# Kernel optimization log

Hardware: AMD Instinct MI355X
Metric: run time of the kernel (lower is better)

The kernel has to match this reference:

```python
import jax, jax.numpy as jnp
import numpy as np

B = 32        # number of groups (batch.unique())
L = 512       # max_len (equal-size groups in this setup)
E = 512       # embed_dim
H = 8         # num_heads
N = B * L


def setup_inputs() -> dict:
    key = jax.random.key(0)
    k1, k2, k3 = jax.random.split(key, 3)
    embeddings = jax.random.normal(k1, (N, E), dtype=jnp.float32)
    # sorted group ids; equal group sizes keep max_len static for jit
    batch = jnp.repeat(jnp.arange(B, dtype=jnp.int32), L)
    in_proj_w = jax.random.normal(k2, (3 * E, E), dtype=jnp.float32) * (1.0 / np.sqrt(E))
    in_proj_b = jnp.zeros((3 * E,), dtype=jnp.float32)
    out_proj_w = jax.random.normal(k3, (E, E), dtype=jnp.float32) * (1.0 / np.sqrt(E))
    out_proj_b = jnp.zeros((E,), dtype=jnp.float32)
    return {"embeddings": embeddings, "batch": batch,
            "in_proj_w": in_proj_w, "in_proj_b": in_proj_b,
            "out_proj_w": out_proj_w, "out_proj_b": out_proj_b}


def reference(embeddings, batch, in_proj_w, in_proj_b, out_proj_w, out_proj_b):
    Dh = E // H
    ones = jnp.ones_like(batch, dtype=jnp.int32)
    counts = jax.ops.segment_sum(ones, batch, num_segments=B)          # [B]
    starts = jnp.cumsum(counts) - counts                               # exclusive cumsum
    pos = jnp.arange(N, dtype=jnp.int32) - starts[batch]               # position within group
    # pad ragged -> [B, L, E] (zeros for padding, as in torch code)
    padded = jnp.zeros((B, L, E), dtype=embeddings.dtype).at[batch, pos].set(embeddings)
    # FAITHFUL float attn_mask: +1.0 added to scores outside the valid block
    valid = (jnp.arange(L)[None, :] < counts[:, None]).astype(embeddings.dtype)  # [B, L]
    add_mask = 1.0 - valid[:, :, None] * valid[:, None, :]             # [B, Lq, Lk]

    qkv = padded @ in_proj_w.T + in_proj_b                             # [B, L, 3E]
    q, k, v = jnp.split(qkv, 3, axis=-1)
    q = q.reshape(B, L, H, Dh)
    k = k.reshape(B, L, H, Dh)
    v = v.reshape(B, L, H, Dh)
    scale = 1.0 / np.sqrt(Dh)
    scores = jnp.einsum('bqhd,bkhd->bhqk', q, k) * scale + add_mask[:, None, :, :]
    attn = jax.nn.softmax(scores, axis=-1)
    ctx = jnp.einsum('bhqk,bkhd->bqhd', attn, v).reshape(B, L, E)
    attn_out = ctx @ out_proj_w.T + out_proj_b                         # [B, L, E]
    # max_pool1d over sequence (includes padded query rows, as original)
    return jnp.max(attn_out, axis=1)                                   # [B, E]
```

## Files before the change

kernel.cpp:

```cpp
#include <hip/hip_runtime.h>
#include <math.h>


#define B_ 32
#define L_ 512
#define E_ 512
#define H_ 8
#define DH 64
#define N_ (B_ * L_)
#define EMB_N (N_ * E_)
#define IPW_N (3 * E_ * E_)
#define OPW_N (E_ * E_)

typedef _Float16 f16;
typedef __attribute__((ext_vector_type(8))) _Float16 f16x8;
typedef __attribute__((ext_vector_type(4))) float f32x4;
typedef unsigned short u16;

__device__ __forceinline__ u16 f16_bits(float x) {
    f16 h = (f16)x;
    return *reinterpret_cast<u16*>(&h);
}
__device__ __forceinline__ unsigned pk2(float a, float b) {
    return (unsigned)f16_bits(a) | ((unsigned)f16_bits(b) << 16);
}
__device__ __forceinline__ unsigned pkrtz(float a, float b) {
    auto r = __builtin_amdgcn_cvt_pkrtz(a, b);
    return *reinterpret_cast<unsigned*>(&r);
}
__device__ __forceinline__ void async16(const void* g, void* l) {
    __builtin_amdgcn_global_load_lds(
        (const __attribute__((address_space(1))) void*)g,
        (__attribute__((address_space(3))) void*)l, 16, 0, 0);
}

__device__ __forceinline__ void atomicMaxFloat(float* addr, float val) {
    if (val >= 0.0f) atomicMax((int*)addr, __float_as_int(val));
    else             atomicMin((unsigned int*)addr, __float_as_uint(val));
}

__global__ __launch_bounds__(256) void cvt_kernel(
        const float* __restrict__ emb, const float* __restrict__ ipw,
        const float* __restrict__ opw,
        u16* __restrict__ eh, u16* __restrict__ wh, u16* __restrict__ oh,
        float* __restrict__ out) {
    if (blockIdx.x < 16) {
        int o = blockIdx.x * 1024 + threadIdx.x * 4;
        float4 ninf = make_float4(-INFINITY, -INFINITY, -INFINITY, -INFINITY);
        *(float4*)(out + o) = ninf;
    }
    size_t i = ((size_t)blockIdx.x * 256 + threadIdx.x) * 8;
    const float* src; u16* dst; size_t off;
    if (i < EMB_N)              { src = emb; dst = eh; off = i; }
    else if (i < EMB_N + IPW_N) { src = ipw; dst = wh; off = i - EMB_N; }
    else                        { src = opw; dst = oh; off = i - EMB_N - IPW_N; }
    float4 a = *(const float4*)(src + off);
    float4 b = *(const float4*)(src + off + 4);
    uint4 p;
    p.x = pk2(a.x, a.y); p.y = pk2(a.z, a.w);
    p.z = pk2(b.x, b.y); p.w = pk2(b.z, b.w);
    *(uint4*)(dst + off) = p;
}

__global__ __launch_bounds__(512) void qkv_mfma(
        const u16* __restrict__ Wg, const u16* __restrict__ Eg,
        const float* __restrict__ bias,
        u16* __restrict__ qg, u16* __restrict__ kg, u16* __restrict__ vg) {
    __shared__ u16 Ah[2][128 * 32];
    __shared__ u16 Bh[2][256 * 32];
    const int tok0 = blockIdx.x * 256, row0 = blockIdx.y * 128;
    const int tid = threadIdx.x, wave = tid >> 6, lane = tid & 63;
    const int quad = lane >> 4, c = lane & 15;
    const int ww = wave & 1, wt = wave >> 1;
    const int sw = (quad ^ ((c >> 1) & 3)) * 8;
    const bool vblk = (row0 >= 1024);

    f32x4 zero = {0.f, 0.f, 0.f, 0.f};
    f32x4 acc[4][4];
#pragma unroll
    for (int i = 0; i < 4; i++)
#pragma unroll
        for (int j = 0; j < 4; j++) acc[i][j] = zero;

    auto stage = [&](int buf, int kt) {
        {
            int chunk = wave * 64 + lane;
            int r = chunk >> 2, g = chunk & 3;
            int pos = g ^ ((r >> 1) & 3);
            async16(Wg + (size_t)(row0 + r) * E_ + kt * 32 + pos * 8,
                    &Ah[buf][wave * 512]);
        }
#pragma unroll
        for (int it = 0; it < 2; it++) {
            int chunk = (it * 8 + wave) * 64 + lane;
            int r = chunk >> 2, g = chunk & 3;
            int pos = g ^ ((r >> 1) & 3);
            async16(Eg + (size_t)(tok0 + r) * E_ + kt * 32 + pos * 8,
                    &Bh[buf][(it * 8 + wave) * 512]);
        }
    };

    stage(0, 0);
    for (int kt = 0; kt < 16; kt++) {
        __syncthreads();
        if (kt < 15) stage((kt + 1) & 1, kt + 1);
        const int buf = kt & 1;
        f16x8 mf[4], nf[4];
        if (!vblk) {
#pragma unroll
            for (int i = 0; i < 4; i++)
                mf[i] = *(const f16x8*)&Ah[buf][(ww * 64 + i * 16 + c) * 32 + sw];
#pragma unroll
            for (int j = 0; j < 4; j++)
                nf[j] = *(const f16x8*)&Bh[buf][(wt * 64 + j * 16 + c) * 32 + sw];
        } else {
#pragma unroll
            for (int i = 0; i < 4; i++)
                mf[i] = *(const f16x8*)&Bh[buf][(wt * 64 + i * 16 + c) * 32 + sw];
#pragma unroll
            for (int j = 0; j < 4; j++)
                nf[j] = *(const f16x8*)&Ah[buf][(ww * 64 + j * 16 + c) * 32 + sw];
        }
#pragma unroll
        for (int i = 0; i < 4; i++)
#pragma unroll
            for (int j = 0; j < 4; j++)
                acc[i][j] = __builtin_amdgcn_mfma_f32_16x16x32_f16(mf[i], nf[j], acc[i][j], 0, 0, 0);
    }

    if (!vblk) {
        const int which = row0 >> 9;
        u16* dst = which ? kg : qg;
        const float scale = which ? 1.0f : 0.18033688f;
        const int h = (((row0 & 511) + ww * 64) >> 6);
#pragma unroll
        for (int i = 0; i < 4; i++) {
            const int d0 = i * 16 + quad * 4;
            float4 bv = *(const float4*)(bias + row0 + ww * 64 + d0);
            const int dch = i * 2 + (quad >> 1);
#pragma unroll
            for (int j = 0; j < 4; j++) {
                int n = tok0 + wt * 64 + j * 16 + c;
                int bb = n >> 9, l = n & 511;
                uint2 st;
                st.x = pk2((acc[i][j][0] + bv.x) * scale, (acc[i][j][1] + bv.y) * scale);
                st.y = pk2((acc[i][j][2] + bv.z) * scale, (acc[i][j][3] + bv.w) * scale);
                size_t addr = (size_t)(bb * H_ + h) * 32768 +
                              (l >> 4) * 1024 + dch * 128 + (l & 15) * 8 + (quad & 1) * 4;
                *(uint2*)(dst + addr) = st;
            }
        }
    } else {
        const int bb = tok0 >> 9;
        const int l0 = (tok0 & 511) + wt * 64;
        const int tt = l0 >> 6;
        const int h = (((row0 & 511) + ww * 64) >> 6);
#pragma unroll
        for (int j = 0; j < 4; j++) {
            int mw = row0 + ww * 64 + j * 16 + c;
            int d = mw & 63;
            float bv = bias[mw];
#pragma unroll
            for (int i = 0; i < 4; i++) {
                uint2 st;
                st.x = pk2(acc[i][j][0] + bv, acc[i][j][1] + bv);
                st.y = pk2(acc[i][j][2] + bv, acc[i][j][3] + bv);
                size_t addr = (size_t)(bb * H_ + h) * 32768 + tt * 4096 +
                              j * 1024 + (i * 2 + (quad >> 1)) * 128 +
                              c * 8 + (quad & 1) * 4;
                *(uint2*)(vg + addr) = st;
            }
        }
    }
}

__global__ __launch_bounds__(256) void attn_mfma(
        const u16* __restrict__ qg, const u16* __restrict__ kg,
        const u16* __restrict__ vg, u16* __restrict__ ctx) {
    __shared__ u16 ps[4][8 * 136];
    const int qt = blockIdx.x, h = blockIdx.y, b = blockIdx.z;
    const int tid = threadIdx.x, wave = tid >> 6, lane = tid & 63;
    const int quad = lane >> 4, c = lane & 15;
    const size_t base = (size_t)(b * H_ + h) * 32768;
    const int lane8 = lane * 8;

    f16x8 qf[2][2];
#pragma unroll
    for (int rs = 0; rs < 2; rs++) {
        const size_t qb = base + (size_t)(qt * 8 + wave * 2 + rs) * 1024;
#pragma unroll
        for (int kk = 0; kk < 2; kk++)
            qf[rs][kk] = *(const f16x8*)(qg + qb + kk * 512 + lane8);
    }

    f32x4 zero = {0.f, 0.f, 0.f, 0.f};
    const f32x4 m6 = {-6.f, -6.f, -6.f, -6.f};
    f16x8 ones;
#pragma unroll
    for (int i = 0; i < 8; i++) ones[i] = (f16)1.0f;

    f32x4 Of[2][4];
    f32x4 lacc[2];
#pragma unroll
    for (int rs = 0; rs < 2; rs++) {
        lacc[rs] = zero;
#pragma unroll
        for (int j = 0; j < 4; j++) Of[rs][j] = zero;
    }

    for (int kt = 0; kt < 8; kt++) {
        const size_t tb = base + (size_t)kt * 4096;
        f16x8 kf[4][2];
#pragma unroll
        for (int jj = 0; jj < 4; jj++)
#pragma unroll
            for (int kk = 0; kk < 2; kk++)
                kf[jj][kk] = *(const f16x8*)(kg + tb + jj * 1024 + kk * 512 + lane8);
        f16x8 vf[2][4];
#pragma unroll
        for (int kk = 0; kk < 2; kk++)
#pragma unroll
            for (int j = 0; j < 4; j++)
                vf[kk][j] = *(const f16x8*)(vg + tb + j * 1024 + kk * 512 + lane8);

#pragma unroll
        for (int rs = 0; rs < 2; rs++) {
            f32x4 Sf[4];
#pragma unroll
            for (int jj = 0; jj < 4; jj++) {
                Sf[jj] = m6;
#pragma unroll
                for (int kk = 0; kk < 2; kk++)
                    Sf[jj] = __builtin_amdgcn_mfma_f32_16x16x32_f16(kf[jj][kk], qf[rs][kk], Sf[jj], 0, 0, 0);
            }
            u16* psw = ps[wave];
#pragma unroll
            for (int jj = 0; jj < 4; jj++) {
                float p0 = exp2f(Sf[jj][0]), p1 = exp2f(Sf[jj][1]);
                float p2 = exp2f(Sf[jj][2]), p3 = exp2f(Sf[jj][3]);
                int addr = (2 * jj + (quad >> 1)) * 136 + c * 8 + 4 * (quad & 1);
                *(uint2*)&psw[addr] = make_uint2(pkrtz(p0, p1), pkrtz(p2, p3));
            }
            f16x8 pf0 = *(const f16x8*)&psw[(0 + quad) * 136 + c * 8];
            f16x8 pf1 = *(const f16x8*)&psw[(4 + quad) * 136 + c * 8];
            lacc[rs] = __builtin_amdgcn_mfma_f32_16x16x32_f16(ones, pf0, lacc[rs], 0, 0, 0);
            lacc[rs] = __builtin_amdgcn_mfma_f32_16x16x32_f16(ones, pf1, lacc[rs], 0, 0, 0);
#pragma unroll
            for (int j = 0; j < 4; j++) {
                Of[rs][j] = __builtin_amdgcn_mfma_f32_16x16x32_f16(vf[0][j], pf0, Of[rs][j], 0, 0, 0);
                Of[rs][j] = __builtin_amdgcn_mfma_f32_16x16x32_f16(vf[1][j], pf1, Of[rs][j], 0, 0, 0);
            }
        }
    }

#pragma unroll
    for (int rs = 0; rs < 2; rs++) {
        float inv = 1.0f / lacc[rs][0];
        int n = b * L_ + qt * 128 + wave * 32 + rs * 16 + c;
#pragma unroll
        for (int j = 0; j < 4; j++) {
            int d0 = j * 16 + quad * 4;
            uint2 st;
            st.x = pk2(Of[rs][j][0] * inv, Of[rs][j][1] * inv);
            st.y = pk2(Of[rs][j][2] * inv, Of[rs][j][3] * inv);
            *(uint2*)(ctx + (size_t)n * E_ + h * DH + d0) = st;
        }
    }
}

__global__ __launch_bounds__(256) void proj_mfma(
        const u16* __restrict__ Ag, const u16* __restrict__ Bg,
        const float* __restrict__ bias, float* __restrict__ out) {
    __shared__ u16 Ah[2][128 * 32], Bh[2][128 * 32];
    __shared__ float red[2][128];
    const int row0 = blockIdx.x * 128, col0 = blockIdx.y * 128;
    const int tid = threadIdx.x, wave = tid >> 6, lane = tid & 63;
    const int quad = lane >> 4, c = lane & 15;
    const int wr = (wave >> 1) * 64, wc = (wave & 1) * 64;
    const int sw = (quad ^ ((c >> 1) & 3)) * 8;

    f32x4 zero = {0.f, 0.f, 0.f, 0.f};
    f32x4 acc[4][4];
#pragma unroll
    for (int i = 0; i < 4; i++)
#pragma unroll
        for (int j = 0; j < 4; j++) acc[i][j] = zero;

    auto stage = [&](int buf, int kt) {
#pragma unroll
        for (int it = 0; it < 2; it++) {
            int chunk = (wave * 2 + it) * 64 + lane;
            int r = chunk >> 2, g = chunk & 3;
            int pos = g ^ ((r >> 1) & 3);
            int lbase = (wave * 2 + it) * 512;
            async16(Ag + (size_t)(row0 + r) * E_ + kt * 32 + pos * 8, &Ah[buf][lbase]);
            async16(Bg + (size_t)(col0 + r) * E_ + kt * 32 + pos * 8, &Bh[buf][lbase]);
        }
    };

    stage(0, 0);
    for (int kt = 0; kt < 16; kt++) {
        __syncthreads();
        if (kt < 15) stage((kt + 1) & 1, kt + 1);
        const int buf = kt & 1;
        f16x8 af[4], bf[4];
#pragma unroll
        for (int i = 0; i < 4; i++)
            af[i] = *(const f16x8*)&Ah[buf][(wr + i * 16 + c) * 32 + sw];
#pragma unroll
        for (int j = 0; j < 4; j++)
            bf[j] = *(const f16x8*)&Bh[buf][(wc + j * 16 + c) * 32 + sw];
#pragma unroll
        for (int i = 0; i < 4; i++)
#pragma unroll
            for (int j = 0; j < 4; j++)
                acc[i][j] = __builtin_amdgcn_mfma_f32_16x16x32_f16(af[i], bf[j], acc[i][j], 0, 0, 0);
    }

    float cm[4];
#pragma unroll
    for (int j = 0; j < 4; j++) {
        cm[j] = -INFINITY;
#pragma unroll
        for (int i = 0; i < 4; i++)
#pragma unroll
            for (int r = 0; r < 4; r++) cm[j] = fmaxf(cm[j], acc[i][j][r]);
        cm[j] = fmaxf(cm[j], __shfl_xor(cm[j], 16));
        cm[j] = fmaxf(cm[j], __shfl_xor(cm[j], 32));
    }
    if (quad == 0)
#pragma unroll
        for (int j = 0; j < 4; j++) red[wave >> 1][wc + j * 16 + c] = cm[j];
    __syncthreads();
    if (tid < 128) {
        int bb = row0 >> 9;
        float m = fmaxf(red[0][tid], red[1][tid]) + bias[col0 + tid];
        atomicMaxFloat(&out[(size_t)bb * E_ + col0 + tid], m);
    }
}

extern "C" void kernel_launch(void* const* d_in, const int* in_sizes, int n_in,
                              void* d_out, int out_size, void* d_ws, size_t ws_size,
                              hipStream_t stream) {
    const float* emb = (const float*)d_in[0];
    const float* ipw = (const float*)d_in[2];
    const float* ipb = (const float*)d_in[3];
    const float* opw = (const float*)d_in[4];
    const float* opb = (const float*)d_in[5];
    float* out = (float*)d_out;

    u16* eh  = (u16*)d_ws;
    u16* wh  = eh + EMB_N;
    u16* oh  = wh + IPW_N;
    u16* qg  = oh + OPW_N;
    u16* kg  = qg + (size_t)N_ * E_;
    u16* vg  = kg + (size_t)N_ * E_;
    u16* ctx = vg + (size_t)N_ * E_;

    cvt_kernel<<<(EMB_N + IPW_N + OPW_N) / (256 * 8), 256, 0, stream>>>(
        emb, ipw, opw, eh, wh, oh, out);
    qkv_mfma<<<dim3(N_ / 256, (3 * E_) / 128), 512, 0, stream>>>(
        wh, eh, ipb, qg, kg, vg);
    attn_mfma<<<dim3(L_ / 128, H_, B_), 256, 0, stream>>>(qg, kg, vg, ctx);
    proj_mfma<<<dim3(N_ / 128, E_ / 128), 256, 0, stream>>>(ctx, oh, opb, out);
}
```

Baseline: 165.0 us.

## Double-buffer K/V register loads in attention and raise MFMA priority

The attention kernel now prefetches the next key tile's K and V fragments into a second register buffer while the current tile is being computed, so global-load latency overlaps with MFMA work. The per-wave LDS staging buffer for P is split by parity and row-set so consecutive writes do not reuse the same region. s_setprio is raised around MFMA blocks and launch bounds request two blocks per SM. The double buffering roughly doubles the K/V register footprint, which risks spills or lower occupancy, and LDS use grows fourfold.

```diff
diff --git a/kernel.cpp b/kernel.cpp
--- a/kernel.cpp
+++ b/kernel.cpp
@@ -174,10 +174,10 @@
     }
 }
 
-__global__ __launch_bounds__(256) void attn_mfma(
+__global__ __launch_bounds__(256, 2) void attn_mfma(
         const u16* __restrict__ qg, const u16* __restrict__ kg,
         const u16* __restrict__ vg, u16* __restrict__ ctx) {
-    __shared__ u16 ps[4][8 * 136];
+    __shared__ u16 ps[4][2][2][1088];
     const int qt = blockIdx.x, h = blockIdx.y, b = blockIdx.z;
     const int tid = threadIdx.x, wave = tid >> 6, lane = tid & 63;
     const int quad = lane >> 4, c = lane & 15;
@@ -208,32 +208,48 @@
         for (int j = 0; j < 4; j++) Of[rs][j] = zero;
     }
 
+    f16x8 kf[2][4][2], vf[2][2][4];
+#pragma unroll
+    for (int jj = 0; jj < 4; jj++)
+#pragma unroll
+        for (int kk = 0; kk < 2; kk++)
+            kf[0][jj][kk] = *(const f16x8*)(kg + base + jj * 1024 + kk * 512 + lane8);
+#pragma unroll
+    for (int kk = 0; kk < 2; kk++)
+#pragma unroll
+        for (int j = 0; j < 4; j++)
+            vf[0][kk][j] = *(const f16x8*)(vg + base + j * 1024 + kk * 512 + lane8);
+
+#pragma unroll
     for (int kt = 0; kt < 8; kt++) {
-        const size_t tb = base + (size_t)kt * 4096;
-        f16x8 kf[4][2];
-#pragma unroll
-        for (int jj = 0; jj < 4; jj++)
+        const int cur = kt & 1, nx = cur ^ 1;
+        if (kt < 7) {
+            const size_t tbn = base + (size_t)(kt + 1) * 4096;
+#pragma unroll
+            for (int jj = 0; jj < 4; jj++)
+#pragma unroll
+                for (int kk = 0; kk < 2; kk++)
+                    kf[nx][jj][kk] = *(const f16x8*)(kg + tbn + jj * 1024 + kk * 512 + lane8);
 #pragma unroll
             for (int kk = 0; kk < 2; kk++)
-                kf[jj][kk] = *(const f16x8*)(kg + tb + jj * 1024 + kk * 512 + lane8);
-        f16x8 vf[2][4];
-#pragma unroll
-        for (int kk = 0; kk < 2; kk++)
-#pragma unroll
-            for (int j = 0; j < 4; j++)
-                vf[kk][j] = *(const f16x8*)(vg + tb + j * 1024 + kk * 512 + lane8);
+#pragma unroll
+                for (int j = 0; j < 4; j++)
+                    vf[nx][kk][j] = *(const f16x8*)(vg + tbn + j * 1024 + kk * 512 + lane8);
+        }
 
 #pragma unroll
         for (int rs = 0; rs < 2; rs++) {
             f32x4 Sf[4];
+            __builtin_amdgcn_s_setprio(1);
 #pragma unroll
             for (int jj = 0; jj < 4; jj++) {
                 Sf[jj] = m6;
 #pragma unroll
                 for (int kk = 0; kk < 2; kk++)
-                    Sf[jj] = __builtin_amdgcn_mfma_f32_16x16x32_f16(kf[jj][kk], qf[rs][kk], Sf[jj], 0, 0, 0);
-            }
-            u16* psw = ps[wave];
+                    Sf[jj] = __builtin_amdgcn_mfma_f32_16x16x32_f16(kf[cur][jj][kk], qf[rs][kk], Sf[jj], 0, 0, 0);
+            }
+            __builtin_amdgcn_s_setprio(0);
+            u16* psw = &ps[wave][cur][rs][0];
 #pragma unroll
             for (int jj = 0; jj < 4; jj++) {
                 float p0 = exp2f(Sf[jj][0]), p1 = exp2f(Sf[jj][1]);
@@ -243,13 +259,15 @@
             }
             f16x8 pf0 = *(const f16x8*)&psw[(0 + quad) * 136 + c * 8];
             f16x8 pf1 = *(const f16x8*)&psw[(4 + quad) * 136 + c * 8];
+            __builtin_amdgcn_s_setprio(1);
             lacc[rs] = __builtin_amdgcn_mfma_f32_16x16x32_f16(ones, pf0, lacc[rs], 0, 0, 0);
             lacc[rs] = __builtin_amdgcn_mfma_f32_16x16x32_f16(ones, pf1, lacc[rs], 0, 0, 0);
 #pragma unroll
             for (int j = 0; j < 4; j++) {
-                Of[rs][j] = __builtin_amdgcn_mfma_f32_16x16x32_f16(vf[0][j], pf0, Of[rs][j], 0, 0, 0);
-                Of[rs][j] = __builtin_amdgcn_mfma_f32_16x16x32_f16(vf[1][j], pf1, Of[rs][j], 0, 0, 0);
-            }
+                Of[rs][j] = __builtin_amdgcn_mfma_f32_16x16x32_f16(vf[cur][0][j], pf0, Of[rs][j], 0, 0, 0);
+                Of[rs][j] = __builtin_amdgcn_mfma_f32_16x16x32_f16(vf[cur][1][j], pf1, Of[rs][j], 0, 0, 0);
+            }
+            __builtin_amdgcn_s_setprio(0);
         }
     }
 
```

Result: faster. 161.7 us (-2.0%).
